# Performance work log

Hardware: AMD Instinct MI355X
Metric: run time of the kernel (lower is better)

## Reference

```python
import jax, jax.numpy as jnp
import numpy as np

N_HEADS = 8
DIM_HEAD = 64
SCALE = DIM_HEAD ** -0.5


def setup_inputs() -> dict:
    key = jax.random.key(0)
    ks = jax.random.split(key, 7)
    B, C, H, W = 2, 512, 64, 64
    inner = N_HEADS * DIM_HEAD  # 512
    x = jax.random.normal(ks[0], (B, C, H, W), dtype=jnp.float32)
    context = jax.random.normal(ks[1], (B, C, H, W), dtype=jnp.float32)
    # kaiming_normal fan_out for 1x1 conv: std = sqrt(2 / out_channels)
    std_qkv = (2.0 / inner) ** 0.5
    std_o = (2.0 / C) ** 0.5
    Wq = jax.random.normal(ks[2], (inner, C), dtype=jnp.float32) * std_qkv
    Wk = jax.random.normal(ks[3], (inner, C), dtype=jnp.float32) * std_qkv
    Wv = jax.random.normal(ks[4], (inner, C), dtype=jnp.float32) * std_qkv
    Wo = jax.random.normal(ks[5], (C, inner), dtype=jnp.float32) * std_o
    return {
        'x': x, 'context': context,
        'Wq': Wq, 'bq': jnp.zeros((inner,), jnp.float32),
        'Wk': Wk, 'bk': jnp.zeros((inner,), jnp.float32),
        'Wv': Wv, 'bv': jnp.zeros((inner,), jnp.float32),
        'Wo': Wo, 'bo': jnp.zeros((C,), jnp.float32),
    }


def _attention(x, context, Wq, bq, Wk, bk, Wv, bv, Wo, bo):
    b, c, h, w = x.shape
    s = h * w
    # 1x1 conv == per-pixel channel matmul. Flatten spatial: [b, s, c]
    xf = x.reshape(b, c, s).transpose(0, 2, 1)
    cf = context.reshape(b, c, s).transpose(0, 2, 1)
    q = jnp.einsum('bsc,ec->bse', xf, Wq) + bq  # [b, s, inner]
    k = jnp.einsum('bsc,ec->bse', cf, Wk) + bk
    v = jnp.einsum('bsc,ec->bse', cf, Wv) + bv
    # split heads: [b, n, s, d]
    def split(t):
        return t.reshape(b, s, N_HEADS, DIM_HEAD).transpose(0, 2, 1, 3)
    q, k, v = split(q), split(k), split(v)
    sim = jnp.einsum('bnid,bnjd->bnij', q, k) * SCALE  # [b, n, s, s]
    attn = jax.nn.softmax(sim, axis=-1)
    out = jnp.einsum('bnij,bnjd->bnid', attn, v)  # [b, n, s, d]
    # merge heads back to channels: 'b n s d -> b (n d) s'
    out = out.transpose(0, 2, 1, 3).reshape(b, s, N_HEADS * DIM_HEAD)
    out = jnp.einsum('bse,ce->bsc', out, Wo) + bo  # output proj (1x1 conv)
    return out.transpose(0, 2, 1).reshape(b, c, h, w)


def reference(x, context, Wq, bq, Wk, bk, Wv, bv, Wo, bo):
    return _attention(x, context, Wq, bq, Wk, bk, Wv, bv, Wo, bo)
```

## Files before the change

### kernel.cpp

```cpp
#include <hip/hip_runtime.h>
#include <cstdint>


typedef __bf16 bf16x8 __attribute__((ext_vector_type(8)));
typedef __bf16 bf16x4 __attribute__((ext_vector_type(4)));
typedef float f32x4 __attribute__((ext_vector_type(4)));
typedef unsigned short u16x8 __attribute__((ext_vector_type(8)));
typedef unsigned short u16x4 __attribute__((ext_vector_type(4)));

#define AS1 __attribute__((address_space(1)))
#define AS3 __attribute__((address_space(3)))

__device__ __forceinline__ void async16(const void* g, void* l) {
  __builtin_amdgcn_global_load_lds((const AS1 void*)g, (AS3 void*)l, 16, 0, 0);
}

__device__ __forceinline__ uint16_t f2bf(float f) {
  union { float f; uint32_t u; } a;
  a.f = f;
  uint32_t r = a.u + 0x7fffu + ((a.u >> 16) & 1u);
  return (uint16_t)(r >> 16);
}

__device__ __forceinline__ float bf2f(uint16_t u) {
  union { uint32_t u; float f; } a;
  a.u = (uint32_t)u << 16;
  return a.f;
}

__global__ __launch_bounds__(256) void cvt_w(
    const float* __restrict__ W0, const float* __restrict__ W1,
    const float* __restrict__ W2, const float* __restrict__ W3,
    uint16_t* __restrict__ O0, uint16_t* __restrict__ O1,
    uint16_t* __restrict__ O2, uint16_t* __restrict__ O3) {
  const float* W[4] = {W0, W1, W2, W3};
  uint16_t* O[4] = {O0, O1, O2, O3};
  const int w = blockIdx.y;
  const int i = (blockIdx.x * 256 + threadIdx.x) * 4;
  float4 v = *(const float4*)&W[w][i];
  u16x4 o = {f2bf(v.x), f2bf(v.y), f2bf(v.z), f2bf(v.w)};
  *(u16x4*)&O[w][i] = o;
}

__global__ __launch_bounds__(256) void transpose_cs(
    const float* __restrict__ x, const float* __restrict__ ctx,
    uint16_t* __restrict__ xT, uint16_t* __restrict__ cT) {
  const int zz = blockIdx.z;
  const float* src = (zz < 2 ? x : ctx) + (size_t)(zz & 1) * 512 * 4096;
  uint16_t* dst = (zz < 2 ? xT : cT) + (size_t)(zz & 1) * 4096 * 512;
  const int s0 = blockIdx.x * 64, c0 = blockIdx.y * 64;
  __shared__ uint16_t tile[64][80];
  const int t = threadIdx.x;
  for (int p = 0; p < 2; ++p) {
    int u = p * 256 + t;
    int r = u >> 3, cg = (u & 7) * 8;
    const float* sp = &src[(size_t)(c0 + r) * 4096 + s0 + cg];
    float4 v0 = *(const float4*)sp;
    float4 v1 = *(const float4*)(sp + 4);
    u16x8 o = {f2bf(v0.x), f2bf(v0.y), f2bf(v0.z), f2bf(v0.w),
               f2bf(v1.x), f2bf(v1.y), f2bf(v1.z), f2bf(v1.w)};
    *(u16x8*)&tile[r][cg] = o;
  }
  __syncthreads();
  for (int p = 0; p < 2; ++p) {
    int u = p * 256 + t;
    int sr = u >> 3, cg = (u & 7) * 8;
    u16x8 v;
    for (int j = 0; j < 8; ++j) v[j] = tile[cg + j][sr];
    *(u16x8*)&dst[(size_t)(s0 + sr) * 512 + c0 + cg] = v;
  }
}

struct QkvArgs {
  const uint16_t* A[3]; long long sA[3];
  const uint16_t* B[3]; long long sB[3];
  uint16_t* C[3];       long long sC[3];
  const float* bias[3];
  float os[3];
  long long ldC[3]; int lx[3]; int brow[3];
};

__global__ __launch_bounds__(256) void gemm_qkv(QkvArgs ga) {
  constexpr int K = 512;
  __shared__ uint16_t At[128 * 32];
  __shared__ uint16_t Bt[128 * 32];
  const int t = threadIdx.x, lane = t & 63, wave = t >> 6;
  const int lr = lane & 15, lq = lane >> 4;
  const int wm = (wave >> 1) * 64, wn = (wave & 1) * 64;
  const int sel = blockIdx.z >> 1, bat = blockIdx.z & 1;
  const int lx = ga.lx[sel], brow = ga.brow[sel];
  const long long ldC = ga.ldC[sel];
  const float os = ga.os[sel];
  const int n0 = (blockIdx.x & ((1 << lx) - 1)) * 128;
  const int m0 = (blockIdx.x >> lx) * 128;
  const uint16_t* A = ga.A[sel] + (size_t)bat * ga.sA[sel];
  const uint16_t* B = ga.B[sel] + (size_t)bat * ga.sB[sel];
  const float* bias = ga.bias[sel];
  f32x4 acc[4][4] = {};
  for (int k0 = 0; k0 < K; k0 += 32) {
    __syncthreads();
    for (int p = 0; p < 2; ++p) {
      int u = p * 256 + t;
      int r = u >> 2, c = (u & 3) * 8;
      async16(&A[(size_t)(m0 + r) * K + k0 + c], &At[p * 2048 + wave * 512]);
      async16(&B[(size_t)(n0 + r) * K + k0 + c], &Bt[p * 2048 + wave * 512]);
    }
    __builtin_amdgcn_s_waitcnt(0);
    __syncthreads();
    bf16x8 af[4], bfr[4];
    for (int i = 0; i < 4; ++i)
      af[i] = *(const bf16x8*)&At[(wm + i * 16 + lr) * 32 + lq * 8];
    for (int j = 0; j < 4; ++j)
      bfr[j] = *(const bf16x8*)&Bt[(wn + j * 16 + lr) * 32 + lq * 8];
    for (int i = 0; i < 4; ++i)
      for (int j = 0; j < 4; ++j)
        acc[i][j] = __builtin_amdgcn_mfma_f32_16x16x32_bf16(af[i], bfr[j], acc[i][j], 0, 0, 0);
  }
  uint16_t* C = ga.C[sel] + (size_t)bat * ga.sC[sel];
  for (int i = 0; i < 4; ++i)
    for (int j = 0; j < 4; ++j) {
      int row = m0 + wm + i * 16 + lq * 4;
      int col = n0 + wn + j * 16 + lr;
      float bc = brow ? 0.f : bias[col];
      u16x4 o;
      for (int r = 0; r < 4; ++r) {
        float val = (acc[i][j][r] + (brow ? bias[row + r] : bc)) * os;
        o[r] = f2bf(val);
      }
      *(u16x4*)&C[(size_t)col * ldC + row] = o;
    }
}

__global__ __launch_bounds__(256) void gemm_out(
    const uint16_t* __restrict__ Ob, long long sA,
    const uint16_t* __restrict__ Wo, float* __restrict__ Y, long long sC,
    const float* __restrict__ bias) {
  constexpr int K = 512;
  __shared__ uint16_t At[128 * 32];
  __shared__ uint16_t Bt[64 * 32];
  const int t = threadIdx.x, lane = t & 63, wave = t >> 6;
  const int lr = lane & 15, lq = lane >> 4;
  const int wm = (wave & 1) * 64, wn = (wave >> 1) * 32;
  const int m0 = blockIdx.y * 128, n0 = blockIdx.x * 64;
  const uint16_t* A = Ob + (size_t)blockIdx.z * sA;
  f32x4 acc[4][2] = {};
  for (int k0 = 0; k0 < K; k0 += 32) {
    __syncthreads();
    for (int p = 0; p < 2; ++p) {
      int u = p * 256 + t;
      int r = u >> 2, c = (u & 3) * 8;
      async16(&A[(size_t)(m0 + r) * K + k0 + c], &At[p * 2048 + wave * 512]);
    }
    {
      int r = t >> 2, c = (t & 3) * 8;
      async16(&Wo[(size_t)(n0 + r) * K + k0 + c], &Bt[wave * 512]);
    }
    __builtin_amdgcn_s_waitcnt(0);
    __syncthreads();
    bf16x8 af[4], bfr[2];
    for (int i = 0; i < 4; ++i)
      af[i] = *(const bf16x8*)&At[(wm + i * 16 + lr) * 32 + lq * 8];
    for (int j = 0; j < 2; ++j)
      bfr[j] = *(const bf16x8*)&Bt[(wn + j * 16 + lr) * 32 + lq * 8];
    for (int i = 0; i < 4; ++i)
      for (int j = 0; j < 2; ++j)
        acc[i][j] = __builtin_amdgcn_mfma_f32_16x16x32_bf16(af[i], bfr[j], acc[i][j], 0, 0, 0);
  }
  float* Cf = Y + (size_t)blockIdx.z * sC;
  for (int i = 0; i < 4; ++i)
    for (int j = 0; j < 2; ++j) {
      int row = m0 + wm + i * 16 + lq * 4;
      int col = n0 + wn + j * 16 + lr;
      float bb = bias[col];
      float4 o = {acc[i][j][0] + bb, acc[i][j][1] + bb,
                  acc[i][j][2] + bb, acc[i][j][3] + bb};
      *(float4*)&Cf[(size_t)col * 4096 + row] = o;
    }
}

__global__ __launch_bounds__(512, 4) void attn128(
    const uint16_t* __restrict__ Q, const uint16_t* __restrict__ K,
    const uint16_t* __restrict__ Vt, uint16_t* __restrict__ Ap,
    float* __restrict__ Lp) {
  constexpr int S = 4096, E = 512;
  const int b = blockIdx.z & 1, jh = blockIdx.z >> 1;
  const int h = blockIdx.y;
  const int i0 = blockIdx.x * 256;
  const int t = threadIdx.x, lane = t & 63, wave = t >> 6;
  const int lr = lane & 15, lq = lane >> 4;
  const size_t qkB = (size_t)b * S * E;
  const size_t vB = (size_t)b * E * S;
  __shared__ uint16_t Kl[4][64 * 64];
  __shared__ uint16_t Vl[4][64 * 64];

  const int qbase = i0 + wave * 32;
  bf16x8 qf[2][2];
  for (int g = 0; g < 2; ++g) {
    const size_t qo = qkB + (size_t)(qbase + g * 16 + lr) * E + h * 64 + lq * 8;
    qf[g][0] = *(const bf16x8*)&Q[qo];
    qf[g][1] = *(const bf16x8*)&Q[qo + 32];
  }
  f32x4 lsum[2] = {};
  f32x4 accOT[2][4] = {};
  const f32x4 fz = {0.f, 0.f, 0.f, 0.f};
  const int swz = (lr & 7);
  const int srr = t >> 3, ssc = ((t & 7) ^ (srr & 7)) * 8;

  const int jbeg = jh * (S / 2), jend = jbeg + S / 2;

  auto stage = [&](int j0, int buf) {
    async16(&K[qkB + (size_t)(j0 + srr) * E + h * 64 + ssc], &Kl[buf][wave * 512]);
    async16(&Vt[vB + (size_t)(h * 64 + srr) * S + j0 + ssc], &Vl[buf][wave * 512]);
  };

  auto do_tile = [&](const uint16_t* Kc, const uint16_t* Vc) {
    f32x4 svt[2][4];
    const int c0 = (lq ^ swz) * 8;
    __builtin_amdgcn_s_setprio(1);
#pragma unroll
    for (int jn = 0; jn < 4; ++jn) {
      const int row = jn * 16 + lr;
      bf16x8 ka0 = *(const bf16x8*)&Kc[row * 64 + c0];
      bf16x8 ka1 = *(const bf16x8*)&Kc[row * 64 + (c0 ^ 32)];
#pragma unroll
      for (int g = 0; g < 2; ++g) {
        f32x4 z = __builtin_amdgcn_mfma_f32_16x16x32_bf16(ka0, qf[g][0], fz, 0, 0, 0);
        z = __builtin_amdgcn_mfma_f32_16x16x32_bf16(ka1, qf[g][1], z, 0, 0, 0);
        svt[g][jn] = z;
      }
    }
    __builtin_amdgcn_s_setprio(0);
    bf16x8 pa[2][2];
#pragma unroll
    for (int g = 0; g < 2; ++g) {
      uint32_t pk[4][2];
#pragma unroll
      for (int jn = 0; jn < 4; ++jn) {
        f32x4 p;
#pragma unroll
        for (int r = 0; r < 4; ++r) p[r] = __builtin_amdgcn_exp2f(svt[g][jn][r]);
        lsum[g] += p;
        asm("v_cvt_pk_bf16_f32 %0, %1, %2" : "=v"(pk[jn][0]) : "v"(p[0]), "v"(p[1]));
        asm("v_cvt_pk_bf16_f32 %0, %1, %2" : "=v"(pk[jn][1]) : "v"(p[2]), "v"(p[3]));
      }
#pragma unroll
      for (int half = 0; half < 2; ++half) {
        union { uint32_t w[4]; bf16x8 v; } f;
#pragma unroll
        for (int p_ = 0; p_ < 2; ++p_) {
          uint32_t a = pk[2 * half][p_];
          uint32_t c = pk[2 * half + 1][p_];
          asm("v_permlane32_swap_b32 %0, %1" : "+v"(a), "+v"(c));
          asm("v_permlane16_swap_b32 %0, %1" : "+v"(a), "+v"(c));
          f.w[p_] = a;
          f.w[2 + p_] = c;
        }
        pa[g][half] = f.v;
      }
    }
    __builtin_amdgcn_s_setprio(1);
#pragma unroll
    for (int dn = 0; dn < 4; ++dn) {
      const int row = dn * 16 + lr;
      bf16x8 v0 = *(const bf16x8*)&Vc[row * 64 + c0];
      bf16x8 v1 = *(const bf16x8*)&Vc[row * 64 + (c0 ^ 32)];
#pragma unroll
      for (int g = 0; g < 2; ++g) {
        accOT[g][dn] = __builtin_amdgcn_mfma_f32_16x16x32_bf16(v0, pa[g][0], accOT[g][dn], 0, 0, 0);
        accOT[g][dn] = __builtin_amdgcn_mfma_f32_16x16x32_bf16(v1, pa[g][1], accOT[g][dn], 0, 0, 0);
      }
    }
    __builtin_amdgcn_s_setprio(0);
  };

  stage(jbeg, 0);
  stage(jbeg + 64, 1);
  __builtin_amdgcn_s_waitcnt(0);
  __syncthreads();

  int nb = 0;
  for (int jp = jbeg; jp < jend; jp += 128) {
    if (jp + 128 < jend) {
      stage(jp + 128, nb ^ 2);
      stage(jp + 192, (nb ^ 2) + 1);
    }
    do_tile(Kl[nb], Vl[nb]);
    do_tile(Kl[nb + 1], Vl[nb + 1]);
    __builtin_amdgcn_s_waitcnt(0);
    __syncthreads();
    nb ^= 2;
  }
  uint16_t* Aph = Ap + (size_t)jh * 2 * S * E;
  float* Lph = Lp + ((size_t)(jh * 2 + b) * 8 + h) * S;
  for (int g = 0; g < 2; ++g) {
    float lt = (lsum[g][0] + lsum[g][1]) + (lsum[g][2] + lsum[g][3]);
    lt += __shfl_xor(lt, 16);
    lt += __shfl_xor(lt, 32);
    if (lane < 16) Lph[qbase + g * 16 + lr] = lt;
    const size_t row = qbase + g * 16 + lr;
    for (int dn = 0; dn < 4; ++dn) {
      u16x4 o;
      for (int r = 0; r < 4; ++r) o[r] = f2bf(accOT[g][dn][r]);
      *(u16x4*)&Aph[qkB + row * E + h * 64 + dn * 16 + lq * 4] = o;
    }
  }
}

__global__ __launch_bounds__(256) void attn_combine(
    const uint16_t* __restrict__ Ap, const float* __restrict__ Lp,
    uint16_t* __restrict__ Ob) {
  constexpr int S = 4096, E = 512;
  const size_t HALF = (size_t)2 * S * E;
  const size_t idx = ((size_t)blockIdx.x * 256 + threadIdx.x) * 4;
  const int b = (int)(idx / ((size_t)S * E));
  const size_t rem = idx % ((size_t)S * E);
  const int s = (int)(rem / E), e = (int)(rem % E);
  const int h = e >> 6;
  const float l0 = Lp[((size_t)(0 * 2 + b) * 8 + h) * S + s];
  const float l1 = Lp[((size_t)(1 * 2 + b) * 8 + h) * S + s];
  const float inv = 1.f / (l0 + l1);
  u16x4 a0 = *(const u16x4*)&Ap[idx];
  u16x4 a1 = *(const u16x4*)&Ap[HALF + idx];
  u16x4 o;
  for (int r = 0; r < 4; ++r) o[r] = f2bf((bf2f(a0[r]) + bf2f(a1[r])) * inv);
  *(u16x4*)&Ob[idx] = o;
}

extern "C" void kernel_launch(void* const* d_in, const int* in_sizes, int n_in,
                              void* d_out, int out_size, void* d_ws, size_t ws_size,
                              hipStream_t stream) {
  const float* x   = (const float*)d_in[0];
  const float* ctx = (const float*)d_in[1];
  const float* Wq  = (const float*)d_in[2];
  const float* bq  = (const float*)d_in[3];
  const float* Wk  = (const float*)d_in[4];
  const float* bk  = (const float*)d_in[5];
  const float* Wv  = (const float*)d_in[6];
  const float* bv  = (const float*)d_in[7];
  const float* Wo  = (const float*)d_in[8];
  const float* bo  = (const float*)d_in[9];
  float* out = (float*)d_out;

  const size_t SZ = (size_t)2 * 4096 * 512;
  uint16_t* xT = (uint16_t*)d_ws;
  uint16_t* cT = xT + SZ;
  uint16_t* Qb = cT + SZ;
  uint16_t* Kb = Qb + SZ;
  uint16_t* Vb = Kb + SZ;
  uint16_t* Ob = Vb + SZ;
  uint16_t* Wqb = Ob + SZ;
  uint16_t* Wkb = Wqb + 512 * 512;
  uint16_t* Wvb = Wkb + 512 * 512;
  uint16_t* Wob = Wvb + 512 * 512;
  uint16_t* Ap  = Wob + 512 * 512;
  float*    Lp  = (float*)(Ap + 2 * SZ);
  const long long sIn = 4096LL * 512LL;
  const float slh = 0.125f * 1.44269504088896f;

  cvt_w<<<dim3(256, 4), 256, 0, stream>>>(Wq, Wk, Wv, Wo, Wqb, Wkb, Wvb, Wob);
  transpose_cs<<<dim3(64, 8, 4), 256, 0, stream>>>(x, ctx, xT, cT);
  QkvArgs qkv = {
      {Wqb, Wkb, cT}, {0, 0, sIn},
      {xT, cT, Wvb}, {sIn, sIn, 0},
      {Qb, Kb, Vb}, {sIn, sIn, sIn},
      {bq, bk, bv},
      {slh, 1.f, 1.f},
      {512, 512, 4096},
      {5, 5, 2},
      {1, 1, 0}};
  gemm_qkv<<<dim3(128, 1, 6), 256, 0, stream>>>(qkv);
  attn128<<<dim3(16, 8, 4), 512, 0, stream>>>(Qb, Kb, Vb, Ap, Lp);
  attn_combine<<<dim3(4096), 256, 0, stream>>>(Ap, Lp, Ob);
  gemm_out<<<dim3(8, 32, 2), 256, 0, stream>>>(Ob, sIn, Wob, out, sIn, bo);
}
```

Baseline: 224.2 us.

## Switch attention kernel to 32x32x16 MFMA and compute row sums via ones-MFMA

Rewrites the attention inner loop to use 32x32x16 bf16 MFMA instructions instead of 16x16x32, which changes the Q fragment layout, the LDS read pattern for K and V, and the permlane shuffles used to build P operands. The softmax row sum is now accumulated with an extra MFMA against a ones vector rather than with VALU adds and cross-lane shuffles. The aim is fewer MFMA issues per tile and less VALU work, at the cost of four extra MFMAs per tile for the sum and a different register footprint under launch_bounds(512,4).

Measured after the change: 230.2 us. +2.7%, slower.

```diff
diff --git a/kernel.cpp b/kernel.cpp
--- a/kernel.cpp
+++ b/kernel.cpp
@@ -5,6 +5,7 @@
 typedef __bf16 bf16x8 __attribute__((ext_vector_type(8)));
 typedef __bf16 bf16x4 __attribute__((ext_vector_type(4)));
 typedef float f32x4 __attribute__((ext_vector_type(4)));
+typedef float f32x16 __attribute__((ext_vector_type(16)));
 typedef unsigned short u16x8 __attribute__((ext_vector_type(8)));
 typedef unsigned short u16x4 __attribute__((ext_vector_type(4)));
 
@@ -187,23 +188,26 @@
   const int h = blockIdx.y;
   const int i0 = blockIdx.x * 256;
   const int t = threadIdx.x, lane = t & 63, wave = t >> 6;
-  const int lr = lane & 15, lq = lane >> 4;
+  const int i31 = lane & 31, hh = lane >> 5, l7 = lane & 7;
   const size_t qkB = (size_t)b * S * E;
   const size_t vB = (size_t)b * E * S;
   __shared__ uint16_t Kl[4][64 * 64];
   __shared__ uint16_t Vl[4][64 * 64];
 
   const int qbase = i0 + wave * 32;
-  bf16x8 qf[2][2];
-  for (int g = 0; g < 2; ++g) {
-    const size_t qo = qkB + (size_t)(qbase + g * 16 + lr) * E + h * 64 + lq * 8;
-    qf[g][0] = *(const bf16x8*)&Q[qo];
-    qf[g][1] = *(const bf16x8*)&Q[qo + 32];
-  }
-  f32x4 lsum[2] = {};
-  f32x4 accOT[2][4] = {};
-  const f32x4 fz = {0.f, 0.f, 0.f, 0.f};
-  const int swz = (lr & 7);
+  bf16x8 qf[4];
+  for (int ks = 0; ks < 4; ++ks)
+    qf[ks] = *(const bf16x8*)&Q[qkB + (size_t)(qbase + i31) * E + h * 64 + ks * 16 + hh * 8];
+
+  union { u16x8 u; bf16x8 v; } onesu;
+  for (int i = 0; i < 8; ++i) onesu.u[i] = 0x3F80;
+  const bf16x8 ones = onesu.v;
+  f32x16 lacc32 = {0.f, 0.f, 0.f, 0.f, 0.f, 0.f, 0.f, 0.f,
+                   0.f, 0.f, 0.f, 0.f, 0.f, 0.f, 0.f, 0.f};
+  f32x16 accOT32[2];
+  accOT32[0] = lacc32;
+  accOT32[1] = lacc32;
+  const f32x16 fz16 = lacc32;
   const int srr = t >> 3, ssc = ((t & 7) ^ (srr & 7)) * 8;
 
   const int jbeg = jh * (S / 2), jend = jbeg + S / 2;
@@ -214,60 +218,49 @@
   };
 
   auto do_tile = [&](const uint16_t* Kc, const uint16_t* Vc) {
-    f32x4 svt[2][4];
-    const int c0 = (lq ^ swz) * 8;
+    uint32_t W[2][8];
+#pragma unroll
+    for (int jt = 0; jt < 2; ++jt) {
+      f32x16 s = fz16;
+      __builtin_amdgcn_s_setprio(1);
+#pragma unroll
+      for (int ks = 0; ks < 4; ++ks) {
+        bf16x8 ka = *(const bf16x8*)&Kc[(jt * 32 + i31) * 64 + ((2 * ks + hh) ^ l7) * 8];
+        s = __builtin_amdgcn_mfma_f32_32x32x16_bf16(ka, qf[ks], s, 0, 0, 0);
+      }
+      __builtin_amdgcn_s_setprio(0);
+#pragma unroll
+      for (int u = 0; u < 8; ++u) {
+        float p0 = __builtin_amdgcn_exp2f(s[2 * u]);
+        float p1 = __builtin_amdgcn_exp2f(s[2 * u + 1]);
+        asm("v_cvt_pk_bf16_f32 %0, %1, %2" : "=v"(W[jt][u]) : "v"(p0), "v"(p1));
+      }
+    }
+    bf16x8 pa[4];
+#pragma unroll
+    for (int js = 0; js < 4; ++js) {
+      const int jt = js >> 1, u0 = (js & 1) * 4;
+      uint32_t a0 = W[jt][u0 + 0], a2 = W[jt][u0 + 2];
+      uint32_t a1 = W[jt][u0 + 1], a3 = W[jt][u0 + 3];
+      asm("v_permlane32_swap_b32 %0, %1" : "+v"(a0), "+v"(a2));
+      asm("v_permlane32_swap_b32 %0, %1" : "+v"(a1), "+v"(a3));
+      union { uint32_t w[4]; bf16x8 v; } f;
+      f.w[0] = a0;
+      f.w[1] = a1;
+      f.w[2] = a2;
+      f.w[3] = a3;
+      pa[js] = f.v;
+    }
+#pragma unroll
+    for (int js = 0; js < 4; ++js)
+      lacc32 = __builtin_amdgcn_mfma_f32_32x32x16_bf16(ones, pa[js], lacc32, 0, 0, 0);
     __builtin_amdgcn_s_setprio(1);
 #pragma unroll
-    for (int jn = 0; jn < 4; ++jn) {
-      const int row = jn * 16 + lr;
-      bf16x8 ka0 = *(const bf16x8*)&Kc[row * 64 + c0];
-      bf16x8 ka1 = *(const bf16x8*)&Kc[row * 64 + (c0 ^ 32)];
-#pragma unroll
-      for (int g = 0; g < 2; ++g) {
-        f32x4 z = __builtin_amdgcn_mfma_f32_16x16x32_bf16(ka0, qf[g][0], fz, 0, 0, 0);
-        z = __builtin_amdgcn_mfma_f32_16x16x32_bf16(ka1, qf[g][1], z, 0, 0, 0);
-        svt[g][jn] = z;
-      }
-    }
-    __builtin_amdgcn_s_setprio(0);
-    bf16x8 pa[2][2];
-#pragma unroll
-    for (int g = 0; g < 2; ++g) {
-      uint32_t pk[4][2];
-#pragma unroll
-      for (int jn = 0; jn < 4; ++jn) {
-        f32x4 p;
-#pragma unroll
-        for (int r = 0; r < 4; ++r) p[r] = __builtin_amdgcn_exp2f(svt[g][jn][r]);
-        lsum[g] += p;
-        asm("v_cvt_pk_bf16_f32 %0, %1, %2" : "=v"(pk[jn][0]) : "v"(p[0]), "v"(p[1]));
-        asm("v_cvt_pk_bf16_f32 %0, %1, %2" : "=v"(pk[jn][1]) : "v"(p[2]), "v"(p[3]));
-      }
-#pragma unroll
-      for (int half = 0; half < 2; ++half) {
-        union { uint32_t w[4]; bf16x8 v; } f;
-#pragma unroll
-        for (int p_ = 0; p_ < 2; ++p_) {
-          uint32_t a = pk[2 * half][p_];
-          uint32_t c = pk[2 * half + 1][p_];
-          asm("v_permlane32_swap_b32 %0, %1" : "+v"(a), "+v"(c));
-          asm("v_permlane16_swap_b32 %0, %1" : "+v"(a), "+v"(c));
-          f.w[p_] = a;
-          f.w[2 + p_] = c;
-        }
-        pa[g][half] = f.v;
-      }
-    }
-    __builtin_amdgcn_s_setprio(1);
-#pragma unroll
-    for (int dn = 0; dn < 4; ++dn) {
-      const int row = dn * 16 + lr;
-      bf16x8 v0 = *(const bf16x8*)&Vc[row * 64 + c0];
-      bf16x8 v1 = *(const bf16x8*)&Vc[row * 64 + (c0 ^ 32)];
-#pragma unroll
-      for (int g = 0; g < 2; ++g) {
-        accOT[g][dn] = __builtin_amdgcn_mfma_f32_16x16x32_bf16(v0, pa[g][0], accOT[g][dn], 0, 0, 0);
-        accOT[g][dn] = __builtin_amdgcn_mfma_f32_16x16x32_bf16(v1, pa[g][1], accOT[g][dn], 0, 0, 0);
+    for (int dt = 0; dt < 2; ++dt) {
+#pragma unroll
+      for (int js = 0; js < 4; ++js) {
+        bf16x8 va = *(const bf16x8*)&Vc[(dt * 32 + i31) * 64 + ((2 * js + hh) ^ l7) * 8];
+        accOT32[dt] = __builtin_amdgcn_mfma_f32_32x32x16_bf16(va, pa[js], accOT32[dt], 0, 0, 0);
       }
     }
     __builtin_amdgcn_s_setprio(0);
@@ -292,18 +285,14 @@
   }
   uint16_t* Aph = Ap + (size_t)jh * 2 * S * E;
   float* Lph = Lp + ((size_t)(jh * 2 + b) * 8 + h) * S;
-  for (int g = 0; g < 2; ++g) {
-    float lt = (lsum[g][0] + lsum[g][1]) + (lsum[g][2] + lsum[g][3]);
-    lt += __shfl_xor(lt, 16);
-    lt += __shfl_xor(lt, 32);
-    if (lane < 16) Lph[qbase + g * 16 + lr] = lt;
-    const size_t row = qbase + g * 16 + lr;
-    for (int dn = 0; dn < 4; ++dn) {
+  if (lane < 32) Lph[qbase + lane] = lacc32[0];
+  const size_t row = qbase + i31;
+  for (int dt = 0; dt < 2; ++dt)
+    for (int u = 0; u < 4; ++u) {
       u16x4 o;
-      for (int r = 0; r < 4; ++r) o[r] = f2bf(accOT[g][dn][r]);
-      *(u16x4*)&Aph[qkB + row * E + h * 64 + dn * 16 + lq * 4] = o;
-    }
-  }
+      for (int r = 0; r < 4; ++r) o[r] = f2bf(accOT32[dt][4 * u + r]);
+      *(u16x4*)&Aph[qkB + row * E + h * 64 + dt * 32 + u * 8 + hh * 4] = o;
+    }
 }
 
 __global__ __launch_bounds__(256) void attn_combine(
```
